# Kernel tuning notes

Hardware: AMD Instinct MI355X
Metric: run time of the kernel (lower is better)

Reference implementation:

```python
import jax, jax.numpy as jnp
import numpy as np

SIGMA_DATA = 16.0
ALPHA_BOND = 1.0
BETA_FLEX = 1.0
BETA_REL_L = 4.0
MOL_W = jnp.array([1.0, 5.0, 5.0, 10.0], dtype=jnp.float32)  # protein, dna, rna, ligand
LDDT_THRESH = jnp.array([0.5, 1.0, 2.0, 4.0], dtype=jnp.float32)
N_RES = 128  # max residue id (residue_indices in [0, N_RES))


def _cdist(x):
    # Euclidean pairwise distances without materializing (..., M, M, 3).
    x2 = jnp.sum(x * x, axis=-1)
    d2 = x2[..., :, None] + x2[..., None, :] - 2.0 * jnp.einsum('...id,...jd->...ij', x, x)
    return jnp.sqrt(jnp.maximum(d2, 1e-12))


def setup_inputs() -> dict:
    B, T, M, NB = 2, 8, 1024, 2048
    key = jax.random.key(0)
    ks = jax.random.split(key, 8)
    return {
        'x_pred': jax.random.normal(ks[0], (B, T, M, 3), dtype=jnp.float32),
        'x_gt': jax.random.normal(ks[1], (B, T, M, 3), dtype=jnp.float32),
        'sigma': jax.random.uniform(ks[2], (B, T), dtype=jnp.float32),
        'bond_lengths': jax.random.uniform(ks[3], (B, NB), dtype=jnp.float32),
        'cond_mask': jnp.zeros((B, T), dtype=bool),
        'atom_mask': jnp.ones((B, M), dtype=bool),
        'observed_mask': jnp.ones((B, M), dtype=bool),
        'mol_type_per_atom': jax.random.randint(ks[4], (B, M), 0, 4),
        'residue_indices': jnp.sort(jax.random.randint(ks[5], (B, M), 0, N_RES), axis=-1),
        'bond_indices': jax.random.randint(ks[6], (B, NB, 2), 0, M),
        'bond_mask': jnp.ones((B, NB), dtype=bool),
    }


def _total_loss(x_pred, x_gt, sigma, bond_lengths, cond_mask, atom_mask,
                observed_mask, mol_type_per_atom, residue_indices, bond_indices, bond_mask):
    B, T, M, _ = x_pred.shape
    f32 = jnp.float32
    target = ~cond_mask                      # (B, T) frames that are supervised
    target_f = target.astype(f32)
    valid = atom_mask & observed_mask        # (B, M)
    valid_f = valid.astype(f32)
    mol_w = MOL_W[mol_type_per_atom]         # (B, M)

    # ---- structure loss (EDM-weighted MSE) ----
    sq_err = jnp.sum((x_pred - x_gt) ** 2, axis=-1)                      # (B, T, M)
    n_valid = jnp.maximum(valid_f.sum(-1), 1.0)                          # (B,)
    per_frame = jnp.sum(sq_err * (mol_w * valid_f)[:, None, :], axis=-1) / n_valid[:, None]
    edm_w = (sigma ** 2 + SIGMA_DATA ** 2) / (sigma * SIGMA_DATA + 1e-8) ** 2 * target_f
    l_struct = jnp.sum(edm_w * per_frame) / jnp.maximum(target_f.sum(), 1.0)

    # ---- bond loss ----
    NB = bond_indices.shape[1]
    idx_i = jnp.broadcast_to(bond_indices[..., 0][:, None, :, None], (B, T, NB, 3))
    idx_j = jnp.broadcast_to(bond_indices[..., 1][:, None, :, None], (B, T, NB, 3))
    xi = jnp.take_along_axis(x_pred, idx_i, axis=2)
    xj = jnp.take_along_axis(x_pred, idx_j, axis=2)
    pred_len = jnp.sqrt(jnp.sum((xi - xj) ** 2, axis=-1) + 1e-12)        # (B, T, NB)
    w = target_f[:, :, None] * bond_mask.astype(f32)[:, None, :]
    l_bond = jnp.sum((pred_len - bond_lengths[:, None, :]) ** 2 * w) / jnp.maximum(w.sum(), 1.0)

    # ---- smooth lDDT ----
    d_pred = _cdist(x_pred)                                              # (B, T, M, M)
    d_gt = _cdist(x_gt)
    eye = jnp.eye(M, dtype=bool)
    dmask = ((d_gt < 15.0)
             & valid[:, None, :, None] & valid[:, None, None, :]
             & target[:, :, None, None] & ~eye)
    diff = jnp.abs(d_pred - d_gt)
    score = jax.nn.sigmoid(LDDT_THRESH - diff[..., None]).mean(-1)       # (B, T, M, M)
    n_pairs = jnp.maximum(dmask.astype(f32).sum(), 1.0)
    l_lddt = 1.0 - jnp.sum(score * dmask.astype(f32)) / n_pairs

    # ---- local (intra-residue) flexibility loss, vectorized segment form ----
    fw = target_f / jnp.maximum(target_f.sum(1, keepdims=True), 1.0)     # (B, T)
    mean_p = jnp.einsum('bt,btij->bij', fw, d_pred)
    mean_g = jnp.einsum('bt,btij->bij', fw, d_gt)
    std_p = jnp.sqrt(jnp.einsum('bt,btij->bij', fw, (d_pred - mean_p[:, None]) ** 2) + 1e-8)
    std_g = jnp.sqrt(jnp.einsum('bt,btij->bij', fw, (d_gt - mean_g[:, None]) ** 2) + 1e-8)
    diff_sq = (std_p - std_g) ** 2                                       # (B, M, M)
    triu = jnp.triu(jnp.ones((M, M), dtype=bool), k=1)
    same_res = residue_indices[:, :, None] == residue_indices[:, None, :]
    pmask = (same_res & valid[:, :, None] & valid[:, None, :] & triu).astype(f32)
    seg = jnp.broadcast_to(
        (jnp.arange(B)[:, None] * N_RES + residue_indices)[:, :, None], (B, M, M)).reshape(-1)
    sums = jax.ops.segment_sum((diff_sq * pmask).reshape(-1), seg, num_segments=B * N_RES)
    cnts = jax.ops.segment_sum(pmask.reshape(-1), seg, num_segments=B * N_RES)
    res_ok = cnts > 0.0                      # residue has >= 2 valid atoms
    res_mean = sums / jnp.maximum(cnts, 1.0)
    l_local = jnp.sum(res_mean * res_ok) / jnp.maximum(res_ok.astype(f32).sum(), 1.0)
    l_flex = BETA_REL_L * l_local

    return l_struct + ALPHA_BOND * l_bond + l_lddt + BETA_FLEX * l_flex


def reference(x_pred, x_gt, sigma, bond_lengths, cond_mask, atom_mask,
              observed_mask, mol_type_per_atom, residue_indices, bond_indices, bond_mask):
    return _total_loss(x_pred, x_gt, sigma, bond_lengths, cond_mask, atom_mask,
                       observed_mask, mol_type_per_atom, residue_indices, bond_indices, bond_mask)
```

## Files before the change

### kernel.cpp

```cpp
#include <hip/hip_runtime.h>
#include <math.h>

#define B 2
#define T 8
#define M 1024
#define NB 2048
#define N_RES 128
#define TILE 32
#define NTILES (M / TILE)
#define NTPAIRS (NTILES * (NTILES + 1) / 2)
#define PAIR_BLOCKS (B * NTPAIRS)
#define BOND_BLOCKS ((B * T * NB) / 256)
#define STRUCT_BLOCKS (B * T)
#define NBLK (PAIR_BLOCKS + BOND_BLOCKS + STRUCT_BLOCKS)

#define WS_FLEXS  0
#define WS_FLEXC  256
#define WS_SC     512
#define WS_CT     (512 + PAIR_BLOCKS)
#define WS_BN     (512 + 2 * PAIR_BLOCKS)
#define WS_BD     (512 + 2 * PAIR_BLOCKS + BOND_BLOCKS)
#define WS_ST     (512 + 2 * PAIR_BLOCKS + 2 * BOND_BLOCKS)
#define WS_TOTAL  (512 + 2 * PAIR_BLOCKS + 2 * BOND_BLOCKS + STRUCT_BLOCKS)

#define C_E1 66.35420923125896f
#define C_E2 678.6088038500627f
#define C_E3 2039.5821756957330f
#define C_E4 1808.0424144560632f
#define C_P0 C_E1
#define C_P1 1357.2176077001254f
#define C_P2 6118.7465270871990f
#define C_P3 7232.1696578242530f

__device__ inline float block_reduce(float v, float* smem) {
    int lane = threadIdx.x & 63, wid = threadIdx.x >> 6;
#pragma unroll
    for (int off = 32; off > 0; off >>= 1) v += __shfl_down(v, off, 64);
    __syncthreads();
    if (lane == 0) smem[wid] = v;
    __syncthreads();
    float r = 0.f;
    if (threadIdx.x == 0) {
        for (int i = 0; i < 4; i++) r += smem[i];
    }
    return r;
}

__global__ __launch_bounds__(256) void k_main(
        const float* __restrict__ xp, const float* __restrict__ xg,
        const float* __restrict__ sigma, const float* __restrict__ blen,
        const int* __restrict__ cond, const int* __restrict__ amask,
        const int* __restrict__ omask, const int* __restrict__ mtype,
        const int* __restrict__ resid, const int* __restrict__ bidx,
        const int* __restrict__ bmask, float* __restrict__ ws) {
    __shared__ float red[8], red2[8];
    __shared__ float sI[T][TILE][6];
    __shared__ float sJ[T][TILE][8];
    __shared__ float s_valI[TILE], s_valJ[TILE];
    __shared__ int   s_resI[TILE], s_resJ[TILE];
    __shared__ float pS[4][TILE], pC[4][TILE];

    const int tid = threadIdx.x;
    const int blk = blockIdx.x;

    if (blk < PAIR_BLOCKS) {
        int bb = blk / NTPAIRS;
        int p  = blk % NTPAIRS;
        int ti = 0, rem = p;
        while (rem >= NTILES - ti) { rem -= NTILES - ti; ti++; }
        int tj = ti + rem;

        float fw[T], tg[T];
        float cb = 0.f;
#pragma unroll
        for (int t = 0; t < T; t++) {
            tg[t] = (cond[bb * T + t] == 0) ? 1.f : 0.f;
            cb += tg[t];
        }
        float inv = 1.f / fmaxf(cb, 1.f);
        float S0 = cb * inv;
#pragma unroll
        for (int t = 0; t < T; t++) fw[t] = tg[t] * inv;

#pragma unroll
        for (int it = 0; it < 3; it++) {
            int u = tid + it * 256;
            int g = u / 24, chunk = u - g * 24;
            int t = g >> 2, side = (g >> 1) & 1, arr = g & 1;
            int tau = side ? tj : ti;
            const float* src = (arr ? xg : xp)
                + ((size_t)(bb * T + t) * M + (size_t)tau * TILE) * 3;
            float4 v = ((const float4*)src)[chunk];
            float* dst = side ? &sJ[t][0][0] : &sI[t][0][0];
            int stride = side ? 8 : 6;
            int e = chunk * 4;
            int a = e / 3, c = e - a * 3;
            float vv[4] = {v.x, v.y, v.z, v.w};
#pragma unroll
            for (int q = 0; q < 4; q++) {
                dst[a * stride + c + arr * 3] = vv[q];
                c++;
                if (c == 3) { c = 0; a++; }
            }
        }
        if (tid < TILE) {
            int i = ti * TILE + tid, j = tj * TILE + tid;
            s_valI[tid] = (amask[bb * M + i] && omask[bb * M + i]) ? 1.f : 0.f;
            s_resI[tid] = resid[bb * M + i];
            s_valJ[tid] = (amask[bb * M + j] && omask[bb * M + j]) ? 1.f : 0.f;
            s_resJ[tid] = resid[bb * M + j];
        }
        __syncthreads();

        const bool doflex = (s_resI[TILE - 1] >= s_resJ[0]) &&
                            (s_resJ[TILE - 1] >= s_resI[0]);

        const int ii = tid & 31;
        float ipx[T], ipy[T], ipz[T], igx[T], igy[T], igz[T];
#pragma unroll
        for (int t = 0; t < T; t++) {
            ipx[t] = sI[t][ii][0]; ipy[t] = sI[t][ii][1]; ipz[t] = sI[t][ii][2];
            igx[t] = sI[t][ii][3]; igy[t] = sI[t][ii][4]; igz[t] = sI[t][ii][5];
        }
        const int   gi = ti * TILE + ii;
        const float vI = s_valI[ii];
        const int   rI = s_resI[ii];
        const int jbase = (tid >> 5) * 4;

        float score_sum = 0.f, cnt_sum = 0.f;
        float fsum = 0.f, fcnt = 0.f;
#pragma unroll
        for (int l = 0; l < 4; l++) {
            int jj = jbase + l;
            int gj = tj * TILE + jj;
            float w = (gi < gj) ? vI * s_valJ[jj] : 0.f;
            float S1p = 0.f, S2p = 0.f, S1g = 0.f, S2g = 0.f;
            float isc = 0.f, icnt = 0.f;
#pragma unroll
            for (int t = 0; t < T; t++) {
                float4 a4 = *(const float4*)&sJ[t][jj][0];
                float4 b4 = *(const float4*)&sJ[t][jj][4];
                float dx = ipx[t] - a4.x, dy = ipy[t] - a4.y, dz = ipz[t] - a4.z;
                float d2p = fmaf(dx, dx, fmaf(dy, dy, dz * dz));
                float dp = __builtin_amdgcn_sqrtf(d2p);
                dx = igx[t] - a4.w; dy = igy[t] - b4.x; dz = igz[t] - b4.y;
                float d2g = fmaf(dx, dx, fmaf(dy, dy, dz * dz));
                float dg = __builtin_amdgcn_sqrtf(d2g);
                S1p = fmaf(fw[t], dp, S1p);  S2p = fmaf(fw[t], d2p, S2p);
                S1g = fmaf(fw[t], dg, S1g);  S2g = fmaf(fw[t], d2g, S2g);
                float diff = fabsf(dp - dg);
                float u = __expf(-diff);
                float Pn = fmaf(u, fmaf(u, fmaf(u, C_P3, C_P2), C_P1), C_P0);
                float Qd = fmaf(u, fmaf(u, fmaf(u, fmaf(u, C_E4, C_E3), C_E2), C_E1), 1.f);
                float s4 = u * Pn * __builtin_amdgcn_rcpf(Qd);
                float mk = (dg < 15.f) ? tg[t] : 0.f;
                isc = fmaf(mk, s4, isc);
                icnt += mk;
            }
            score_sum = fmaf(w * 0.25f, isc, score_sum);
            cnt_sum = fmaf(w, icnt, cnt_sum);
            if (doflex && w > 0.f && rI == s_resJ[jj]) {
                float varp = fmaxf(fmaf(-S1p * S1p, 2.f - S0, S2p), 0.f);
                float varg = fmaxf(fmaf(-S1g * S1g, 2.f - S0, S2g), 0.f);
                float ds = __builtin_amdgcn_sqrtf(varp + 1e-8f)
                         - __builtin_amdgcn_sqrtf(varg + 1e-8f);
                fsum = fmaf(ds, ds, fsum);
                fcnt += 1.f;
            }
        }
        float sc = block_reduce(score_sum, red);
        float ct = block_reduce(cnt_sum, red2);
        if (tid == 0) {
            ws[WS_SC + blk] = 2.f * sc;
            ws[WS_CT + blk] = 2.f * ct;
        }

        if (doflex) {
            fsum += __shfl_xor(fsum, 32, 64);
            fcnt += __shfl_xor(fcnt, 32, 64);
            int wv = tid >> 6, lane = tid & 63;
            __syncthreads();
            if (lane < 32) { pS[wv][lane] = fsum; pC[wv][lane] = fcnt; }
            __syncthreads();
            if (tid < 32) {
                float s = pS[0][tid] + pS[1][tid] + pS[2][tid] + pS[3][tid];
                float c = pC[0][tid] + pC[1][tid] + pC[2][tid] + pC[3][tid];
                pS[0][tid] = s; pC[0][tid] = c;
            }
            __syncthreads();
            if (tid < 32) {
                int r = s_resI[tid];
                bool head = (tid == 0) || (s_resI[tid - 1] != r);
                if (head) {
                    float s = 0.f, c = 0.f;
                    for (int k = tid; k < 32 && s_resI[k] == r; k++) {
                        s += pS[0][k]; c += pC[0][k];
                    }
                    if (c > 0.f) {
                        atomicAdd(ws + WS_FLEXS + bb * N_RES + r, s);
                        atomicAdd(ws + WS_FLEXC + bb * N_RES + r, c);
                    }
                }
            }
        }
    } else if (blk < PAIR_BLOCKS + BOND_BLOCKS) {
        int bix = blk - PAIR_BLOCKS;
        int gid = bix * 256 + tid;
        int bb = gid / (T * NB);
        int r  = gid % (T * NB);
        int t = r / NB, k = r % NB;
        float w = ((cond[bb * T + t] == 0) && bmask[bb * NB + k]) ? 1.f : 0.f;
        int i = bidx[(bb * NB + k) * 2 + 0];
        int j = bidx[(bb * NB + k) * 2 + 1];
        const float* base = xp + (size_t)(bb * T + t) * M * 3;
        float dx = base[i * 3 + 0] - base[j * 3 + 0];
        float dy = base[i * 3 + 1] - base[j * 3 + 1];
        float dz = base[i * 3 + 2] - base[j * 3 + 2];
        float len = __builtin_amdgcn_sqrtf(fmaf(dx, dx, fmaf(dy, dy, dz * dz)) + 1e-12f);
        float d = len - blen[bb * NB + k];
        float n  = block_reduce(w * d * d, red);
        float dn = block_reduce(w, red2);
        if (tid == 0) {
            ws[WS_BN + bix] = n;
            ws[WS_BD + bix] = dn;
        }
    } else {
        int bt = blk - PAIR_BLOCKS - BOND_BLOCKS;
        int bb = bt / T, t = bt % T;
        const float* p = xp + (size_t)(bb * T + t) * M * 3;
        const float* g = xg + (size_t)(bb * T + t) * M * 3;
        float lw = 0.f, lv = 0.f;
        for (int m = tid; m < M; m += 256) {
            float v = (amask[bb * M + m] && omask[bb * M + m]) ? 1.f : 0.f;
            lv += v;
            int mt = mtype[bb * M + m];
            float mw = (mt == 0) ? 1.f : ((mt == 3) ? 10.f : 5.f);
            float dx = p[m * 3 + 0] - g[m * 3 + 0];
            float dy = p[m * 3 + 1] - g[m * 3 + 1];
            float dz = p[m * 3 + 2] - g[m * 3 + 2];
            lw += fmaf(dx, dx, fmaf(dy, dy, dz * dz)) * v * mw;
        }
        float tot = block_reduce(lw, red);
        float nv  = block_reduce(lv, red2);
        if (tid == 0) {
            float per_frame = tot / fmaxf(nv, 1.f);
            float s = sigma[bb * T + t];
            float targ = (cond[bb * T + t] == 0) ? 1.f : 0.f;
            float den = s * 16.0f + 1e-8f;
            float edm = (s * s + 256.0f) / (den * den) * targ;
            ws[WS_ST + bt] = edm * per_frame;
        }
    }
}

__global__ void k_final(const float* __restrict__ ws, const int* __restrict__ cond,
                        float* __restrict__ out) {
    __shared__ float red[8], red2[8];
    int tid = threadIdx.x;
    float sc = 0.f, ct = 0.f;
    for (int i = tid; i < PAIR_BLOCKS; i += 256) {
        sc += ws[WS_SC + i];
        ct += ws[WS_CT + i];
    }
    float bn = 0.f, bd = 0.f;
    for (int i = tid; i < BOND_BLOCKS; i += 256) {
        bn += ws[WS_BN + i];
        bd += ws[WS_BD + i];
    }
    float st = (tid < STRUCT_BLOCKS) ? ws[WS_ST + tid] : 0.f;
    float ls = 0.f, ln = 0.f;
    for (int seg = tid; seg < B * N_RES; seg += 256) {
        float c = ws[WS_FLEXC + seg];
        if (c > 0.f) { ls += ws[WS_FLEXS + seg] / c; ln += 1.f; }
    }
    float scs = block_reduce(sc, red);
    float cts = block_reduce(ct, red2);
    float bns = block_reduce(bn, red);
    float bds = block_reduce(bd, red2);
    float sts = block_reduce(st, red);
    float lss = block_reduce(ls, red2);
    float lns = block_reduce(ln, red);
    if (tid == 0) {
        float tc = 0.f;
        for (int i = 0; i < B * T; i++) tc += (cond[i] == 0) ? 1.f : 0.f;
        float l_struct = sts / fmaxf(tc, 1.f);
        float l_bond = bns / fmaxf(bds, 1.f);
        float l_lddt = 1.f - scs / fmaxf(cts, 1.f);
        float l_local = lss / fmaxf(lns, 1.f);
        out[0] = l_struct + l_bond + l_lddt + 4.0f * l_local;
    }
}

extern "C" void kernel_launch(void* const* d_in, const int* in_sizes, int n_in,
                              void* d_out, int out_size, void* d_ws, size_t ws_size,
                              hipStream_t stream) {
    const float* xp    = (const float*)d_in[0];
    const float* xg    = (const float*)d_in[1];
    const float* sigma = (const float*)d_in[2];
    const float* blen  = (const float*)d_in[3];
    const int*   cond  = (const int*)d_in[4];
    const int*   amask = (const int*)d_in[5];
    const int*   omask = (const int*)d_in[6];
    const int*   mtype = (const int*)d_in[7];
    const int*   resid = (const int*)d_in[8];
    const int*   bidx  = (const int*)d_in[9];
    const int*   bmask = (const int*)d_in[10];
    float* out = (float*)d_out;
    float* ws  = (float*)d_ws;

    hipMemsetAsync(ws, 0, 512 * sizeof(float), stream);
    k_main<<<NBLK, 256, 0, stream>>>(xp, xg, sigma, blen, cond, amask, omask,
                                     mtype, resid, bidx, bmask, ws);
    k_final<<<1, 256, 0, stream>>>(ws, cond, out);
}
```

Baseline: 95.50 us.

## Move flex loss into dedicated per-residue blocks and drop memset

Removes the per-frame variance accumulators and flex reduction from the all-pairs LDDT tile loop. Flex terms are now computed by new per-residue blocks that binary-search each residue's atom range and loop only over intra-residue pairs. This lightens register pressure and ALU work in the hot pair loop and removes the atomics and the workspace memset launch. In exchange it adds 256 extra blocks doing uncoalesced global gathers, and each block's work depends on residue size.

```diff
diff --git a/kernel.cpp b/kernel.cpp
--- a/kernel.cpp
+++ b/kernel.cpp
@@ -12,16 +12,17 @@
 #define PAIR_BLOCKS (B * NTPAIRS)
 #define BOND_BLOCKS ((B * T * NB) / 256)
 #define STRUCT_BLOCKS (B * T)
-#define NBLK (PAIR_BLOCKS + BOND_BLOCKS + STRUCT_BLOCKS)
-
-#define WS_FLEXS  0
-#define WS_FLEXC  256
-#define WS_SC     512
-#define WS_CT     (512 + PAIR_BLOCKS)
-#define WS_BN     (512 + 2 * PAIR_BLOCKS)
-#define WS_BD     (512 + 2 * PAIR_BLOCKS + BOND_BLOCKS)
-#define WS_ST     (512 + 2 * PAIR_BLOCKS + 2 * BOND_BLOCKS)
-#define WS_TOTAL  (512 + 2 * PAIR_BLOCKS + 2 * BOND_BLOCKS + STRUCT_BLOCKS)
+#define FLEX_BLOCKS (B * N_RES)
+#define NBLK (PAIR_BLOCKS + BOND_BLOCKS + STRUCT_BLOCKS + FLEX_BLOCKS)
+
+#define WS_SC     0
+#define WS_CT     (WS_SC + PAIR_BLOCKS)
+#define WS_BN     (WS_CT + PAIR_BLOCKS)
+#define WS_BD     (WS_BN + BOND_BLOCKS)
+#define WS_ST     (WS_BD + BOND_BLOCKS)
+#define WS_RM     (WS_ST + STRUCT_BLOCKS)
+#define WS_RO     (WS_RM + FLEX_BLOCKS)
+#define WS_TOTAL  (WS_RO + FLEX_BLOCKS)
 
 #define C_E1 66.35420923125896f
 #define C_E2 678.6088038500627f
@@ -56,9 +57,7 @@
     __shared__ float red[8], red2[8];
     __shared__ float sI[T][TILE][6];
     __shared__ float sJ[T][TILE][8];
-    __shared__ float s_valI[TILE], s_valJ[TILE];
-    __shared__ int   s_resI[TILE], s_resJ[TILE];
-    __shared__ float pS[4][TILE], pC[4][TILE];
+    __shared__ float s_valJ[TILE];
 
     const int tid = threadIdx.x;
     const int blk = blockIdx.x;
@@ -70,17 +69,10 @@
         while (rem >= NTILES - ti) { rem -= NTILES - ti; ti++; }
         int tj = ti + rem;
 
-        float fw[T], tg[T];
-        float cb = 0.f;
-#pragma unroll
-        for (int t = 0; t < T; t++) {
+        float tg[T];
+#pragma unroll
+        for (int t = 0; t < T; t++)
             tg[t] = (cond[bb * T + t] == 0) ? 1.f : 0.f;
-            cb += tg[t];
-        }
-        float inv = 1.f / fmaxf(cb, 1.f);
-        float S0 = cb * inv;
-#pragma unroll
-        for (int t = 0; t < T; t++) fw[t] = tg[t] * inv;
 
 #pragma unroll
         for (int it = 0; it < 3; it++) {
@@ -104,16 +96,10 @@
             }
         }
         if (tid < TILE) {
-            int i = ti * TILE + tid, j = tj * TILE + tid;
-            s_valI[tid] = (amask[bb * M + i] && omask[bb * M + i]) ? 1.f : 0.f;
-            s_resI[tid] = resid[bb * M + i];
+            int j = tj * TILE + tid;
             s_valJ[tid] = (amask[bb * M + j] && omask[bb * M + j]) ? 1.f : 0.f;
-            s_resJ[tid] = resid[bb * M + j];
         }
         __syncthreads();
-
-        const bool doflex = (s_resI[TILE - 1] >= s_resJ[0]) &&
-                            (s_resJ[TILE - 1] >= s_resI[0]);
 
         const int ii = tid & 31;
         float ipx[T], ipy[T], ipz[T], igx[T], igy[T], igz[T];
@@ -123,31 +109,24 @@
             igx[t] = sI[t][ii][3]; igy[t] = sI[t][ii][4]; igz[t] = sI[t][ii][5];
         }
         const int   gi = ti * TILE + ii;
-        const float vI = s_valI[ii];
-        const int   rI = s_resI[ii];
+        const float vI = (amask[bb * M + gi] && omask[bb * M + gi]) ? 1.f : 0.f;
         const int jbase = (tid >> 5) * 4;
 
         float score_sum = 0.f, cnt_sum = 0.f;
-        float fsum = 0.f, fcnt = 0.f;
 #pragma unroll
         for (int l = 0; l < 4; l++) {
             int jj = jbase + l;
             int gj = tj * TILE + jj;
             float w = (gi < gj) ? vI * s_valJ[jj] : 0.f;
-            float S1p = 0.f, S2p = 0.f, S1g = 0.f, S2g = 0.f;
             float isc = 0.f, icnt = 0.f;
 #pragma unroll
             for (int t = 0; t < T; t++) {
                 float4 a4 = *(const float4*)&sJ[t][jj][0];
                 float4 b4 = *(const float4*)&sJ[t][jj][4];
                 float dx = ipx[t] - a4.x, dy = ipy[t] - a4.y, dz = ipz[t] - a4.z;
-                float d2p = fmaf(dx, dx, fmaf(dy, dy, dz * dz));
-                float dp = __builtin_amdgcn_sqrtf(d2p);
+                float dp = __builtin_amdgcn_sqrtf(fmaf(dx, dx, fmaf(dy, dy, dz * dz)));
                 dx = igx[t] - a4.w; dy = igy[t] - b4.x; dz = igz[t] - b4.y;
-                float d2g = fmaf(dx, dx, fmaf(dy, dy, dz * dz));
-                float dg = __builtin_amdgcn_sqrtf(d2g);
-                S1p = fmaf(fw[t], dp, S1p);  S2p = fmaf(fw[t], d2p, S2p);
-                S1g = fmaf(fw[t], dg, S1g);  S2g = fmaf(fw[t], d2g, S2g);
+                float dg = __builtin_amdgcn_sqrtf(fmaf(dx, dx, fmaf(dy, dy, dz * dz)));
                 float diff = fabsf(dp - dg);
                 float u = __expf(-diff);
                 float Pn = fmaf(u, fmaf(u, fmaf(u, C_P3, C_P2), C_P1), C_P0);
@@ -159,49 +138,12 @@
             }
             score_sum = fmaf(w * 0.25f, isc, score_sum);
             cnt_sum = fmaf(w, icnt, cnt_sum);
-            if (doflex && w > 0.f && rI == s_resJ[jj]) {
-                float varp = fmaxf(fmaf(-S1p * S1p, 2.f - S0, S2p), 0.f);
-                float varg = fmaxf(fmaf(-S1g * S1g, 2.f - S0, S2g), 0.f);
-                float ds = __builtin_amdgcn_sqrtf(varp + 1e-8f)
-                         - __builtin_amdgcn_sqrtf(varg + 1e-8f);
-                fsum = fmaf(ds, ds, fsum);
-                fcnt += 1.f;
-            }
         }
         float sc = block_reduce(score_sum, red);
         float ct = block_reduce(cnt_sum, red2);
         if (tid == 0) {
             ws[WS_SC + blk] = 2.f * sc;
             ws[WS_CT + blk] = 2.f * ct;
-        }
-
-        if (doflex) {
-            fsum += __shfl_xor(fsum, 32, 64);
-            fcnt += __shfl_xor(fcnt, 32, 64);
-            int wv = tid >> 6, lane = tid & 63;
-            __syncthreads();
-            if (lane < 32) { pS[wv][lane] = fsum; pC[wv][lane] = fcnt; }
-            __syncthreads();
-            if (tid < 32) {
-                float s = pS[0][tid] + pS[1][tid] + pS[2][tid] + pS[3][tid];
-                float c = pC[0][tid] + pC[1][tid] + pC[2][tid] + pC[3][tid];
-                pS[0][tid] = s; pC[0][tid] = c;
-            }
-            __syncthreads();
-            if (tid < 32) {
-                int r = s_resI[tid];
-                bool head = (tid == 0) || (s_resI[tid - 1] != r);
-                if (head) {
-                    float s = 0.f, c = 0.f;
-                    for (int k = tid; k < 32 && s_resI[k] == r; k++) {
-                        s += pS[0][k]; c += pC[0][k];
-                    }
-                    if (c > 0.f) {
-                        atomicAdd(ws + WS_FLEXS + bb * N_RES + r, s);
-                        atomicAdd(ws + WS_FLEXC + bb * N_RES + r, c);
-                    }
-                }
-            }
         }
     } else if (blk < PAIR_BLOCKS + BOND_BLOCKS) {
         int bix = blk - PAIR_BLOCKS;
@@ -224,7 +166,7 @@
             ws[WS_BN + bix] = n;
             ws[WS_BD + bix] = dn;
         }
-    } else {
+    } else if (blk < PAIR_BLOCKS + BOND_BLOCKS + STRUCT_BLOCKS) {
         int bt = blk - PAIR_BLOCKS - BOND_BLOCKS;
         int bb = bt / T, t = bt % T;
         const float* p = xp + (size_t)(bb * T + t) * M * 3;
@@ -250,6 +192,71 @@
             float edm = (s * s + 256.0f) / (den * den) * targ;
             ws[WS_ST + bt] = edm * per_frame;
         }
+    } else {
+        int bfr = blk - PAIR_BLOCKS - BOND_BLOCKS - STRUCT_BLOCKS;
+        int bb = bfr >> 7, r = bfr & (N_RES - 1);
+        const int* R = resid + bb * M;
+
+        float fw[T];
+        float cb = 0.f;
+#pragma unroll
+        for (int t = 0; t < T; t++) {
+            float g = (cond[bb * T + t] == 0) ? 1.f : 0.f;
+            fw[t] = g; cb += g;
+        }
+        float inv = 1.f / fmaxf(cb, 1.f);
+        float S0 = cb * inv;
+#pragma unroll
+        for (int t = 0; t < T; t++) fw[t] *= inv;
+
+        int lo = 0, hi = M;
+        while (lo < hi) { int mid = (lo + hi) >> 1; if (R[mid] < r) lo = mid + 1; else hi = mid; }
+        int s0 = lo;
+        hi = M;
+        while (lo < hi) { int mid = (lo + hi) >> 1; if (R[mid] <= r) lo = mid + 1; else hi = mid; }
+        int e0 = lo;
+        int k = e0 - s0;
+        int tot = (k * (k - 1)) >> 1;
+
+        float wsum = 0.f, wcnt = 0.f;
+        for (int idx = tid; idx < tot; idx += 256) {
+            int pp = 0, rem = idx;
+            while (rem >= k - 1 - pp) { rem -= k - 1 - pp; pp++; }
+            int ai = s0 + pp, aj = s0 + pp + 1 + rem;
+            float w = ((amask[bb * M + ai] && omask[bb * M + ai]) ? 1.f : 0.f)
+                    * ((amask[bb * M + aj] && omask[bb * M + aj]) ? 1.f : 0.f);
+            float S1p = 0.f, S2p = 0.f, S1g = 0.f, S2g = 0.f;
+#pragma unroll
+            for (int t = 0; t < T; t++) {
+                const float* P = xp + (size_t)(bb * T + t) * M * 3;
+                const float* G = xg + (size_t)(bb * T + t) * M * 3;
+                float dx = P[ai * 3 + 0] - P[aj * 3 + 0];
+                float dy = P[ai * 3 + 1] - P[aj * 3 + 1];
+                float dz = P[ai * 3 + 2] - P[aj * 3 + 2];
+                float d2p = fmaf(dx, dx, fmaf(dy, dy, dz * dz));
+                float dp = __builtin_amdgcn_sqrtf(d2p);
+                dx = G[ai * 3 + 0] - G[aj * 3 + 0];
+                dy = G[ai * 3 + 1] - G[aj * 3 + 1];
+                dz = G[ai * 3 + 2] - G[aj * 3 + 2];
+                float d2g = fmaf(dx, dx, fmaf(dy, dy, dz * dz));
+                float dg = __builtin_amdgcn_sqrtf(d2g);
+                S1p = fmaf(fw[t], dp, S1p);  S2p = fmaf(fw[t], d2p, S2p);
+                S1g = fmaf(fw[t], dg, S1g);  S2g = fmaf(fw[t], d2g, S2g);
+            }
+            float varp = fmaxf(fmaf(-S1p * S1p, 2.f - S0, S2p), 0.f);
+            float varg = fmaxf(fmaf(-S1g * S1g, 2.f - S0, S2g), 0.f);
+            float ds = __builtin_amdgcn_sqrtf(varp + 1e-8f)
+                     - __builtin_amdgcn_sqrtf(varg + 1e-8f);
+            wsum = fmaf(w, ds * ds, wsum);
+            wcnt += w;
+        }
+        float ssum = block_reduce(wsum, red);
+        float scnt = block_reduce(wcnt, red2);
+        if (tid == 0) {
+            float ok = (scnt > 0.f) ? 1.f : 0.f;
+            ws[WS_RM + bfr] = ok * ssum / fmaxf(scnt, 1.f);
+            ws[WS_RO + bfr] = ok;
+        }
     }
 }
 
@@ -268,11 +275,8 @@
         bd += ws[WS_BD + i];
     }
     float st = (tid < STRUCT_BLOCKS) ? ws[WS_ST + tid] : 0.f;
-    float ls = 0.f, ln = 0.f;
-    for (int seg = tid; seg < B * N_RES; seg += 256) {
-        float c = ws[WS_FLEXC + seg];
-        if (c > 0.f) { ls += ws[WS_FLEXS + seg] / c; ln += 1.f; }
-    }
+    float ls = (tid < FLEX_BLOCKS) ? ws[WS_RM + tid] : 0.f;
+    float ln = (tid < FLEX_BLOCKS) ? ws[WS_RO + tid] : 0.f;
     float scs = block_reduce(sc, red);
     float cts = block_reduce(ct, red2);
     float bns = block_reduce(bn, red);
@@ -308,7 +312,6 @@
     float* out = (float*)d_out;
     float* ws  = (float*)d_ws;
 
-    hipMemsetAsync(ws, 0, 512 * sizeof(float), stream);
     k_main<<<NBLK, 256, 0, stream>>>(xp, xg, sigma, blen, cond, amask, omask,
                                      mtype, resid, bidx, bmask, ws);
     k_final<<<1, 256, 0, stream>>>(ws, cond, out);
```

Result: no change. 94.49 us (-1.1%).
